# Optimization experiments

Hardware: AMD Instinct MI355X
Metric: run time of the kernel (lower is better)

Reference implementation:

```python
import jax, jax.numpy as jnp
import numpy as np

B, T, C, H = 4, 2048, 1024, 1024

def setup_inputs() -> dict:
    key = jax.random.key(0)
    ks = jax.random.split(key, 7)
    s = 0.02
    return {
        "x": jax.random.normal(ks[0], (B, T, C), dtype=jnp.float32),
        "k": jax.random.normal(ks[1], (B, T, C), dtype=jnp.float32),
        "q": jax.random.normal(ks[2], (B, T, C), dtype=jnp.float32),
        "v": jax.random.normal(ks[3], (B, T, C), dtype=jnp.float32),
        "Wk": jax.random.normal(ks[4], (C, H), dtype=jnp.float32) * s,
        "Wq": jax.random.normal(ks[5], (C, H), dtype=jnp.float32) * s,
        "Wv": jax.random.normal(ks[6], (C, H), dtype=jnp.float32) * s,
    }

def reference(x, k, q, v, Wk, Wq, Wv):
    Tcur = x.shape[1]
    kp = jnp.einsum('btc,ch->bth', k, Wk)
    qp = jnp.einsum('btc,ch->bth', q, Wq)
    # NOTE: original torch code (faithfully) projects v with the QUERY weights
    vp = jnp.einsum('btc,ch->bth', v, Wq)
    scale = jnp.asarray(H, jnp.float32) ** -0.5
    weights = jnp.einsum('bth,bsh->bts', qp, kp) * scale  # [B,T,T]
    causal = jnp.tril(jnp.ones((Tcur, Tcur), dtype=bool))
    weights = jnp.where(causal, weights, -jnp.inf)
    weights = jax.nn.softmax(weights, axis=-1)
    # dropout p=0.0 -> identity
    out = jnp.einsum('bts,bsh->bth', weights, vp)
    return out
```

## Files before the change

### kernel.cpp

```cpp
#include <hip/hip_runtime.h>
#include <stdint.h>
#include <math.h>

typedef unsigned short u16;
typedef __attribute__((ext_vector_type(8))) short short8;
typedef __attribute__((ext_vector_type(8))) u16 ushort8;
typedef __attribute__((ext_vector_type(4))) u16 u16x4;
typedef __attribute__((ext_vector_type(4))) float floatx4;

__device__ __forceinline__ u16 f2bf(float f) {
  union { float f; unsigned u; } c; c.f = f;
  unsigned u = c.u;
  return (u16)((u + 0x7fffu + ((u >> 16) & 1u)) >> 16);
}
__device__ __forceinline__ float bf2f(u16 h) {
  union { unsigned u; float f; } c; c.u = (unsigned)h << 16;
  return c.f;
}

__device__ __forceinline__ void async16(const u16* g, u16* l) {
  auto* gp = reinterpret_cast<const __attribute__((address_space(1))) uint32_t*>(
      reinterpret_cast<uintptr_t>(g));
  auto* lp = reinterpret_cast<__attribute__((address_space(3))) uint32_t*>(
      reinterpret_cast<uintptr_t>(l));
  __builtin_amdgcn_global_load_lds(gp, lp, 16, 0, 0);
}

#define WAIT_VM4 0xF74
#define WAIT_VM0 0xF70

template <int OUT_BF16>
__global__ __launch_bounds__(256) void gemm_bt(
    const u16* __restrict__ A, const u16* __restrict__ B, void* __restrict__ Cv,
    int K, int lda, int ldb, int ldc,
    long long sA, long long sB, long long sC,
    float scale, int tri_grid, int causal_klimit, int rev_m,
    int vpt, u16* __restrict__ vpC) {
  int bm, bn;
  if (tri_grid) {
    const int bx = blockIdx.x;
    int i = (int)((sqrtf(8.f * bx + 1.f) - 1.f) * 0.5f);
    while ((i + 1) * (i + 2) / 2 <= bx) ++i;
    while (i * (i + 1) / 2 > bx) --i;
    bm = i;
    bn = bx - i * (i + 1) / 2;
  } else {
    bm = rev_m ? ((int)gridDim.x - 1 - (int)blockIdx.x) : (int)blockIdx.x;
    bn = blockIdx.y;
  }
  const int m0 = bm * 128;
  const int n0 = bn * 128;
  A += (size_t)blockIdx.z * sA;
  B += (size_t)blockIdx.z * sB;

  __shared__ u16 As[2][4096];
  __shared__ u16 Bs[2][4096];

  const int tid = threadIdx.x;
  const int lane = tid & 63;
  const int wid = tid >> 6;
  const int wm = (wid & 1) * 64;
  const int wn = (wid >> 1) * 64;
  const int fr = lane & 15;
  const int fq = lane >> 4;

  floatx4 acc[4][4] = {};

  int kt_end = K >> 5;
  if (causal_klimit) {
    int lim = (m0 >> 5) + 4;
    if (lim < kt_end) kt_end = lim;
  }

  const int rowi = tid >> 2;
  const int segi = tid & 3;
  const int sgz = segi ^ ((rowi >> 1) & 3);
  const u16* gA = A + (size_t)(m0 + rowi) * lda + sgz * 8;
  const u16* gB = B + (size_t)(n0 + rowi) * ldb + sgz * 8;

  int offA[4], offB[4];
#pragma unroll
  for (int i = 0; i < 4; ++i) {
    int ra = wm + i * 16 + fr;
    offA[i] = ra * 32 + (fq ^ ((ra >> 1) & 3)) * 8;
    int rb = wn + i * 16 + fr;
    offB[i] = rb * 32 + (fq ^ ((rb >> 1) & 3)) * 8;
  }

  auto issue = [&](int kt) {
    const int k0 = kt << 5;
    const int odd = kt & 1;
    async16(gA + k0, &As[odd][tid * 8]);
    async16(gA + k0 + (size_t)64 * lda, &As[odd][tid * 8 + 2048]);
    async16(gB + k0, &Bs[odd][tid * 8]);
    async16(gB + k0 + (size_t)64 * ldb, &Bs[odd][tid * 8 + 2048]);
  };

  issue(0);
  for (int kt = 0; kt < kt_end; ++kt) {
    if (kt + 1 < kt_end) {
      issue(kt + 1);
      __builtin_amdgcn_s_waitcnt(WAIT_VM4);
    } else {
      __builtin_amdgcn_s_waitcnt(WAIT_VM0);
    }
    asm volatile("s_barrier" ::: "memory");

    const u16* ab = As[kt & 1];
    const u16* bb = Bs[kt & 1];
    short8 av[4], bv[4];
#pragma unroll
    for (int i = 0; i < 4; ++i) av[i] = *(const short8*)(ab + offA[i]);
#pragma unroll
    for (int j = 0; j < 4; ++j) bv[j] = *(const short8*)(bb + offB[j]);

#pragma unroll
    for (int i = 0; i < 4; ++i)
#pragma unroll
      for (int j = 0; j < 4; ++j)
        acc[i][j] = __builtin_amdgcn_mfma_f32_16x16x32_bf16(av[i], bv[j],
                                                            acc[i][j], 0, 0, 0);
    asm volatile("s_barrier" ::: "memory");
  }

  if (vpt && blockIdx.z == 2) {
#pragma unroll
    for (int i = 0; i < 4; ++i) {
      const int m = m0 + wm + i * 16 + fq * 4;
      const int b = m >> 11, t = m & 2047;
#pragma unroll
      for (int j = 0; j < 4; ++j) {
        const int n = n0 + wn + j * 16 + fr;
        u16x4 o;
#pragma unroll
        for (int r = 0; r < 4; ++r) o[r] = f2bf(acc[i][j][r]);
        *(u16x4*)&vpC[(size_t)b * 2097152 + (size_t)n * 2048 + t] = o;
      }
    }
    return;
  }
  if (OUT_BF16) {
    u16* C = (u16*)Cv + (size_t)blockIdx.z * sC;
#pragma unroll
    for (int i = 0; i < 4; ++i) {
      const int m = m0 + wm + i * 16 + fq * 4;
#pragma unroll
      for (int j = 0; j < 4; ++j) {
        const int n = n0 + wn + j * 16 + fr;
#pragma unroll
        for (int r = 0; r < 4; ++r)
          C[(size_t)(m + r) * ldc + n] = f2bf(acc[i][j][r] * scale);
      }
    }
  } else {
    float* C = (float*)Cv + (size_t)blockIdx.z * sC;
#pragma unroll
    for (int i = 0; i < 4; ++i) {
      const int m = m0 + wm + i * 16 + fq * 4;
#pragma unroll
      for (int j = 0; j < 4; ++j) {
        const int n = n0 + wn + j * 16 + fr;
#pragma unroll
        for (int r = 0; r < 4; ++r)
          C[(size_t)(m + r) * ldc + n] = acc[i][j][r] * scale;
      }
    }
  }
}

__global__ __launch_bounds__(256) void cast3(
    const float* __restrict__ q, const float* __restrict__ k,
    const float* __restrict__ v, u16* __restrict__ out, int n8) {
  int i = blockIdx.x * 256 + threadIdx.x;
  if (i >= n8) return;
  const float* src = blockIdx.y == 0 ? q : (blockIdx.y == 1 ? k : v);
  u16* dst = out + (size_t)blockIdx.y * n8 * 8;
  floatx4 a = ((const floatx4*)src)[i * 2];
  floatx4 b = ((const floatx4*)src)[i * 2 + 1];
  ushort8 o;
#pragma unroll
  for (int j = 0; j < 4; ++j) { o[j] = f2bf(a[j]); o[4 + j] = f2bf(b[j]); }
  ((ushort8*)dst)[i] = o;
}

__global__ __launch_bounds__(256) void transpose_castW(
    const float* __restrict__ Wq, const float* __restrict__ Wk,
    u16* __restrict__ out, int R, int C) {
  __shared__ u16 tile[64][72];
  const float* in = (blockIdx.z == 1) ? Wk : Wq;
  u16* dst = out + (size_t)blockIdx.z * R * C;
  const int r0 = blockIdx.x * 64;
  const int c0 = blockIdx.y * 64;
  const int tid = threadIdx.x;
#pragma unroll
  for (int rnd = 0; rnd < 2; ++rnd) {
    int e = rnd * 256 + tid;
    int rr = e >> 3, seg = e & 7;
    const float* p = &in[(size_t)(r0 + rr) * C + c0 + seg * 8];
    floatx4 a = *(const floatx4*)p;
    floatx4 b = *(const floatx4*)(p + 4);
    u16* tp = &tile[rr][seg * 8];
#pragma unroll
    for (int j = 0; j < 4; ++j) { tp[j] = f2bf(a[j]); tp[4 + j] = f2bf(b[j]); }
  }
  __syncthreads();
#pragma unroll
  for (int rnd = 0; rnd < 2; ++rnd) {
    int e = rnd * 256 + tid;
    int cc = e >> 3, rseg = e & 7;
    ushort8 tv;
#pragma unroll
    for (int j = 0; j < 8; ++j) tv[j] = tile[rseg * 8 + j][cc];
    *(ushort8*)&dst[(size_t)(c0 + cc) * R + r0 + rseg * 8] = tv;
  }
}

__global__ __launch_bounds__(256) void softmax_causal(u16* __restrict__ S,
                                                      int T) {
  const int row = blockIdx.x;
  const int t = row & (T - 1);
  const int len = t + 1;
  u16* srow = S + (size_t)row * T;
  const int tid = threadIdx.x;

  float vals[8];
  int cnt = 0;
  float mx = -1e30f;
  for (int i = tid; i < len; i += 256) {
    float v = bf2f(srow[i]);
    vals[cnt++] = v;
    mx = fmaxf(mx, v);
  }
  __shared__ float red[4];
#pragma unroll
  for (int o = 32; o > 0; o >>= 1) mx = fmaxf(mx, __shfl_down(mx, o, 64));
  if ((tid & 63) == 0) red[tid >> 6] = mx;
  __syncthreads();
  mx = fmaxf(fmaxf(red[0], red[1]), fmaxf(red[2], red[3]));
  __syncthreads();

  float sum = 0.f;
  for (int c = 0; c < cnt; ++c) {
    vals[c] = __expf(vals[c] - mx);
    sum += vals[c];
  }
#pragma unroll
  for (int o = 32; o > 0; o >>= 1) sum += __shfl_down(sum, o, 64);
  if ((tid & 63) == 0) red[tid >> 6] = sum;
  __syncthreads();
  sum = red[0] + red[1] + red[2] + red[3];
  const float inv = 1.f / sum;

  int c = 0;
  for (int i = tid; i < len; i += 256) srow[i] = f2bf(vals[c++] * inv);
  for (int i = tid; i < T; i += 256)
    if (i >= len) srow[i] = 0;
}

extern "C" void kernel_launch(void* const* d_in, const int* in_sizes, int n_in,
                              void* d_out, int out_size, void* d_ws,
                              size_t ws_size, hipStream_t stream) {
  (void)in_sizes; (void)n_in; (void)out_size; (void)ws_size;
  const float* k  = (const float*)d_in[1];
  const float* q  = (const float*)d_in[2];
  const float* v  = (const float*)d_in[3];
  const float* Wk = (const float*)d_in[4];
  const float* Wq = (const float*)d_in[5];
  float* out = (float*)d_out;

  const int B = 4, T = 2048, C = 1024, H = 1024;
  const int M = B * T;
  const size_t MC = (size_t)M * C, CH = (size_t)C * H, MH = (size_t)M * H;

  u16* qkv  = (u16*)d_ws;
  u16* WT   = qkv + 3 * MC;
  u16* qkvp = WT + 3 * CH;
  u16* vpT  = qkvp + 2 * MH;
  u16* Sb   = vpT + MH;

  const int n8 = (int)(MC / 8);
  cast3<<<dim3(n8 / 256, 3), 256, 0, stream>>>(q, k, v, qkv, n8);
  transpose_castW<<<dim3(C / 64, H / 64, 3), 256, 0, stream>>>(Wq, Wk, WT, C, H);

  gemm_bt<1><<<dim3(M / 128, H / 128, 3), 256, 0, stream>>>(
      qkv, WT, qkvp, C, C, C, H,
      (long long)MC, (long long)CH, (long long)MH, 1.f, 0, 0, 0, 1, vpT);

  gemm_bt<1><<<dim3(136, 1, B), 256, 0, stream>>>(
      qkvp, qkvp + MH, Sb, H, H, H, T,
      (long long)T * H, (long long)T * H, (long long)T * T,
      0.03125f, 1, 0, 0, 0, nullptr);

  softmax_causal<<<dim3(B * T), 256, 0, stream>>>(Sb, T);

  gemm_bt<0><<<dim3(T / 128, H / 128, B), 256, 0, stream>>>(
      Sb, vpT, out, T, T, T, H,
      (long long)T * T, (long long)H * T, (long long)T * H,
      1.f, 0, 1, 1, 0, nullptr);
}
```

Measured before the change: 332.1 us.

## Use 128x64 tiles with 2-wave blocks for attention GEMMs and vectorize softmax

```diff
diff --git a/kernel.cpp b/kernel.cpp
--- a/kernel.cpp
+++ b/kernel.cpp
@@ -26,35 +26,40 @@
   __builtin_amdgcn_global_load_lds(gp, lp, 16, 0, 0);
 }
 
-#define WAIT_VM4 0xF74
-#define WAIT_VM0 0xF70
-
-template <int OUT_BF16>
-__global__ __launch_bounds__(256) void gemm_bt(
+template <int TAG, int NW, int OUT_BF16>
+__global__ __launch_bounds__(NW * 64) void gemm_bt(
     const u16* __restrict__ A, const u16* __restrict__ B, void* __restrict__ Cv,
     int K, int lda, int ldb, int ldc,
     long long sA, long long sB, long long sC,
     float scale, int tri_grid, int causal_klimit, int rev_m,
     int vpt, u16* __restrict__ vpC) {
+  constexpr int BN = (NW == 4) ? 128 : 64;
+  constexpr int RPR = NW * 16;
+  constexpr int AR = 128 / RPR;
+  constexpr int BR = BN / RPR;
+  constexpr int NLOAD = AR + BR;
+  constexpr int WAIT_KT = 0xF70 | NLOAD;
+  constexpr int WAIT_0 = 0xF70;
+
   int bm, bn;
   if (tri_grid) {
     const int bx = blockIdx.x;
-    int i = (int)((sqrtf(8.f * bx + 1.f) - 1.f) * 0.5f);
-    while ((i + 1) * (i + 2) / 2 <= bx) ++i;
-    while (i * (i + 1) / 2 > bx) --i;
+    int i = (int)sqrtf((float)bx);
+    while ((i + 1) * (i + 2) <= bx) ++i;
+    while (i * (i + 1) > bx) --i;
     bm = i;
-    bn = bx - i * (i + 1) / 2;
+    bn = bx - i * (i + 1);
   } else {
     bm = rev_m ? ((int)gridDim.x - 1 - (int)blockIdx.x) : (int)blockIdx.x;
     bn = blockIdx.y;
   }
   const int m0 = bm * 128;
-  const int n0 = bn * 128;
+  const int n0 = bn * BN;
   A += (size_t)blockIdx.z * sA;
   B += (size_t)blockIdx.z * sB;
 
   __shared__ u16 As[2][4096];
-  __shared__ u16 Bs[2][4096];
+  __shared__ u16 Bs[2][BN * 32];
 
   const int tid = threadIdx.x;
   const int lane = tid & 63;
@@ -90,19 +95,23 @@
   auto issue = [&](int kt) {
     const int k0 = kt << 5;
     const int odd = kt & 1;
-    async16(gA + k0, &As[odd][tid * 8]);
-    async16(gA + k0 + (size_t)64 * lda, &As[odd][tid * 8 + 2048]);
-    async16(gB + k0, &Bs[odd][tid * 8]);
-    async16(gB + k0 + (size_t)64 * ldb, &Bs[odd][tid * 8 + 2048]);
+#pragma unroll
+    for (int r = 0; r < AR; ++r)
+      async16(gA + k0 + (size_t)(r * RPR) * lda,
+              &As[odd][tid * 8 + r * RPR * 32]);
+#pragma unroll
+    for (int r = 0; r < BR; ++r)
+      async16(gB + k0 + (size_t)(r * RPR) * ldb,
+              &Bs[odd][tid * 8 + r * RPR * 32]);
   };
 
   issue(0);
   for (int kt = 0; kt < kt_end; ++kt) {
     if (kt + 1 < kt_end) {
       issue(kt + 1);
-      __builtin_amdgcn_s_waitcnt(WAIT_VM4);
+      __builtin_amdgcn_s_waitcnt(WAIT_KT);
     } else {
-      __builtin_amdgcn_s_waitcnt(WAIT_VM0);
+      __builtin_amdgcn_s_waitcnt(WAIT_0);
     }
     asm volatile("s_barrier" ::: "memory");
 
@@ -222,14 +231,16 @@
   const int len = t + 1;
   u16* srow = S + (size_t)row * T;
   const int tid = threadIdx.x;
-
+  const int base = tid * 8;
+
+  ushort8 v8 = *(const ushort8*)&srow[base];
   float vals[8];
-  int cnt = 0;
   float mx = -1e30f;
-  for (int i = tid; i < len; i += 256) {
-    float v = bf2f(srow[i]);
-    vals[cnt++] = v;
-    mx = fmaxf(mx, v);
+#pragma unroll
+  for (int j = 0; j < 8; ++j) {
+    float x = (base + j < len) ? bf2f(v8[j]) : -1e30f;
+    vals[j] = x;
+    mx = fmaxf(mx, x);
   }
   __shared__ float red[4];
 #pragma unroll
@@ -240,9 +251,11 @@
   __syncthreads();
 
   float sum = 0.f;
-  for (int c = 0; c < cnt; ++c) {
-    vals[c] = __expf(vals[c] - mx);
-    sum += vals[c];
+#pragma unroll
+  for (int j = 0; j < 8; ++j) {
+    float e = (base + j < len) ? __expf(vals[j] - mx) : 0.f;
+    vals[j] = e;
+    sum += e;
   }
 #pragma unroll
   for (int o = 32; o > 0; o >>= 1) sum += __shfl_down(sum, o, 64);
@@ -251,10 +264,10 @@
   sum = red[0] + red[1] + red[2] + red[3];
   const float inv = 1.f / sum;
 
-  int c = 0;
-  for (int i = tid; i < len; i += 256) srow[i] = f2bf(vals[c++] * inv);
-  for (int i = tid; i < T; i += 256)
-    if (i >= len) srow[i] = 0;
+  ushort8 o8;
+#pragma unroll
+  for (int j = 0; j < 8; ++j) o8[j] = f2bf(vals[j] * inv);
+  *(ushort8*)&srow[base] = o8;
 }
 
 extern "C" void kernel_launch(void* const* d_in, const int* in_sizes, int n_in,
@@ -282,18 +295,18 @@
   cast3<<<dim3(n8 / 256, 3), 256, 0, stream>>>(q, k, v, qkv, n8);
   transpose_castW<<<dim3(C / 64, H / 64, 3), 256, 0, stream>>>(Wq, Wk, WT, C, H);
 
-  gemm_bt<1><<<dim3(M / 128, H / 128, 3), 256, 0, stream>>>(
+  gemm_bt<0, 4, 1><<<dim3(M / 128, H / 128, 3), 256, 0, stream>>>(
       qkv, WT, qkvp, C, C, C, H,
       (long long)MC, (long long)CH, (long long)MH, 1.f, 0, 0, 0, 1, vpT);
 
-  gemm_bt<1><<<dim3(136, 1, B), 256, 0, stream>>>(
+  gemm_bt<1, 2, 1><<<dim3(272, 1, B), 128, 0, stream>>>(
       qkvp, qkvp + MH, Sb, H, H, H, T,
       (long long)T * H, (long long)T * H, (long long)T * T,
       0.03125f, 1, 0, 0, 0, nullptr);
 
   softmax_causal<<<dim3(B * T), 256, 0, stream>>>(Sb, T);
 
-  gemm_bt<0><<<dim3(T / 128, H / 128, B), 256, 0, stream>>>(
+  gemm_bt<2, 2, 0><<<dim3(T / 128, H / 64, B), 128, 0, stream>>>(
       Sb, vpT, out, T, T, T, H,
       (long long)T * T, (long long)H * T, (long long)T * H,
       1.f, 0, 1, 1, 0, nullptr);
```

Result: no change. 338.0 us (+1.8%).
